# Kernel tuning notes

Hardware: AMD Instinct MI355X
Metric: run time of the kernel (lower is better)

The kernel has to match this reference:

```python
import jax, jax.numpy as jnp
import numpy as np

CM = 8        # channel_mult
EPS = 1e-5    # BatchNorm eps
NEG = 0.2     # LeakyReLU slope


def conv2d(x, w, stride, pad, b=None):
    y = jax.lax.conv_general_dilated(
        x, w, (stride, stride), [(pad, pad), (pad, pad)],
        dimension_numbers=('NCHW', 'OIHW', 'NCHW'))
    if b is not None:
        y = y + b[None, :, None, None]
    return y


def per_sample_conv(x, w, stride, pad):
    # x: [B,C,H,W], w: [B,O,C,kh,kw] -> per-sample conv, vmapped over batch
    f = lambda xi, wi: conv2d(xi[None], wi, stride, pad)[0]
    return jax.vmap(f)(x, w)


def batchnorm(x, g, b):
    # training-mode BN: batch statistics over (N,H,W)
    m = jnp.mean(x, axis=(0, 2, 3), keepdims=True)
    v = jnp.var(x, axis=(0, 2, 3), keepdims=True)
    return (x - m) * jax.lax.rsqrt(v + EPS) * g[None, :, None, None] + b[None, :, None, None]


def lrelu(x):
    return jnp.where(x >= 0, x, NEG * x)


def setup_inputs() -> dict:
    key = jax.random.key(0)
    ks = jax.random.split(key, 16)
    B, H, W = 16, 512, 512

    def rn(k, shape, fan_in):
        return jax.random.normal(k, shape, jnp.float32) * np.float32(1.0 / np.sqrt(fan_in))

    inp = {}
    inp['x'] = jax.random.normal(ks[0], (B, 3, H, W), jnp.float32)
    n_meta = 3 * (CM // 2) * 25 + CM * (CM * 2 // 2) * 25  # 300 + 1600 = 1900
    inp['conv_weights'] = jax.random.normal(ks[1], (B, n_meta), jnp.float32) * 0.05
    inp['w11'] = rn(ks[2], (CM // 2, 3, 5, 5), 3 * 25)
    inp['b11'] = jnp.zeros((CM // 2,), jnp.float32)
    inp['w12'] = rn(ks[3], (CM * 2 // 2, CM, 5, 5), CM * 25)
    inp['b12'] = jnp.zeros((CM * 2 // 2,), jnp.float32)
    inp['bn1_g'] = jnp.ones((CM * 2,), jnp.float32)
    inp['bn1_b'] = jnp.zeros((CM * 2,), jnp.float32)
    # conv2 stack: (in, out, kernel)
    chans = [(CM * 2, CM * 4, 5), (CM * 4, CM * 8, 5), (CM * 8, CM * 16, 3), (CM * 16, CM * 16, 3)]
    for i, (ci, co, k) in enumerate(chans, 1):
        inp[f'c2w{i}'] = rn(ks[3 + i], (co, ci, k, k), ci * k * k)
        inp[f'c2b{i}'] = jnp.zeros((co,), jnp.float32)
        inp[f'bn{i}g'] = jnp.ones((co,), jnp.float32)
        inp[f'bn{i}b'] = jnp.zeros((co,), jnp.float32)
    return inp


def reference(x, conv_weights, w11, b11, w12, b12, bn1_g, bn1_b,
              c2w1, c2b1, bn1g, bn1b, c2w2, c2b2, bn2g, bn2b,
              c2w3, c2b3, bn3g, bn3b, c2w4, c2b4, bn4g, bn4b):
    B, _, H, W = x.shape
    n1 = 3 * (CM // 2) * 25
    w1 = conv_weights[:, :n1].reshape(B, CM // 2, 3, 5, 5)
    w2 = conv_weights[:, n1:].reshape(B, CM * 2 // 2, CM, 5, 5)

    # meta layer 1: shared half + per-sample dynamic half
    xx = conv2d(x, w11, 1, 2, b11)                  # [B, cm/2, H, W]
    half = per_sample_conv(x, w1, 1, 2)             # [B, cm/2, H, W]
    h = lrelu(jnp.concatenate([xx, half], axis=1))  # [B, cm, H, W]

    # meta layer 2 (stride 2)
    xx = conv2d(h, w12, 2, 2, b12)                  # [B, cm, H/2, W/2]
    half = per_sample_conv(h, w2, 2, 2)             # [B, cm, H/2, W/2]
    h = lrelu(batchnorm(jnp.concatenate([xx, half], axis=1), bn1_g, bn1_b))

    # dense conv stack
    for w_, b_, g_, be_, p in [
        (c2w1, c2b1, bn1g, bn1b, 2),
        (c2w2, c2b2, bn2g, bn2b, 2),
        (c2w3, c2b3, bn3g, bn3b, 1),
        (c2w4, c2b4, bn4g, bn4b, 1),
    ]:
        h = lrelu(batchnorm(conv2d(h, w_, 2, p, b_), g_, be_))

    return h.reshape(-1, CM * 16, H // 32, W // 32)
```

## Files before the change

### kernel.cpp

```cpp
#include <hip/hip_runtime.h>


typedef __attribute__((ext_vector_type(8))) short short8v;
typedef __attribute__((ext_vector_type(4))) float float4v;
typedef __attribute__((ext_vector_type(4))) unsigned short ushort4v;
typedef unsigned short u16;

#define LRELU_NEG 0.2f
#define BN_EPS 1e-5f

__device__ __forceinline__ float bf2f(u16 u){ union{unsigned i; float f;} v; v.i=(unsigned)u<<16; return v.f; }
__device__ __forceinline__ u16 f2bf(float f){ unsigned x=__float_as_uint(f); x += 0x7FFFu + ((x>>16)&1u); return (u16)(x>>16); }
__device__ __forceinline__ float lrelu(float v){ return v<0.f? LRELU_NEG*v : v; }

__device__ __forceinline__ void packw(int i, const float* __restrict__ w, u16* __restrict__ dst,
                                      int IC, int OC, int KSZ, int CPR) {
  int kq = i & 31, oc = (i>>5) % OC, c = i/(OC*32);
  int ky = c / CPR, r = c % CPR;
  int kk = r*32 + kq; int kx = kk / IC, ic = kk % IC;
  float v = (kx < KSZ) ? w[(((size_t)oc*IC + ic)*KSZ + ky)*KSZ + kx] : 0.f;
  dst[i] = f2bf(v);
}

__global__ __launch_bounds__(256) void prep_all(
    const float* __restrict__ w11, const float* __restrict__ w12,
    const float* __restrict__ b12, const float* __restrict__ cw,
    const float* __restrict__ wc1, const float* __restrict__ wc2,
    const float* __restrict__ wc3, const float* __restrict__ wc4,
    u16* __restrict__ wl1d, u16* __restrict__ wl2m, float* __restrict__ bl2,
    u16* __restrict__ d1, u16* __restrict__ d2, u16* __restrict__ d3, u16* __restrict__ d4,
    u16* __restrict__ h1) {
  int i = blockIdx.x*256 + threadIdx.x;
  if (i < 16) {
    bl2[i] = (i<8)? b12[i] : 0.f;
  } else if (i < 49168) {
    int j = i - 16;
    int b = j / 3072, r = j % 3072;
    int c = r >> 9, r2 = r & 511;
    int row = r2 >> 5, kk = r2 & 31;
    int kx = kk >> 2, ic = kk & 3;
    int grp = row >> 3, oc = row & 7;
    int ky = c - grp;
    float v = 0.f;
    if (ic < 3 && kx < 5 && ky >= 0 && ky < 5)
      v = (oc < 4) ? w11[((oc*3+ic)*5+ky)*5+kx]
                   : cw[b*1900 + (oc-4)*75 + ic*25 + ky*5 + kx];
    wl1d[j] = f2bf(v);
  } else if (i < 131088) {
    int j = i - 49168;
    int kq = j & 31, oc = (j>>5) & 15, c = (j>>9) % 10, b = j / 5120;
    int ky = c >> 1, r = c & 1;
    int kk = r*32 + kq; int kx = kk >> 3, ic = kk & 7;
    float v = 0.f;
    if (kx < 5)
      v = (oc < 8) ? w12[((oc*8+ic)*5+ky)*5+kx]
                   : cw[b*1900 + 300 + ((oc-8)*8+ic)*25 + ky*5 + kx];
    wl2m[j] = f2bf(v);
  } else if (i < 196880) {
    int j = i - 131088;
    int b = j / 4112, p = j % 4112;
    int y, xx;
    if (p < 2064) { int r = p/516; y = (r<2)? r : 512+r; xx = p%516; }
    else          { int q = p-2064; int cidx = q&3; xx = (cidx<2)? cidx : 512+cidx; y = 2 + (q>>2); }
    short8v z = {0,0,0,0,0,0,0,0};
    *(short8v*)(h1 + ((((size_t)b*516 + y)*2 + (xx&1))*258 + (xx>>1))*8) = z;
  } else if (i < 484624) {
    int j = i - 196880;
    if (j < 15360) packw(j, wc1, d1, 16, 32, 5, 3);
    else if (j < 66560) packw(j-15360, wc2, d2, 32, 64, 5, 5);
    else if (j < 140288) packw(j-66560, wc3, d3, 64, 128, 3, 6);
    else packw(j-140288, wc4, d4, 128, 128, 3, 12);
  }
}

__global__ __launch_bounds__(256) void conv_l1(const float* __restrict__ x,
    const u16* __restrict__ wl1d, const float* __restrict__ b11,
    u16* __restrict__ h1) {
  __shared__ __align__(16) u16 sx[20*72*4 + 32];
  const int tid = threadIdx.x, b = blockIdx.z;
  const int x0 = (blockIdx.x & 7) * 64;
  const int r0 = (blockIdx.x >> 3) * 16;

  if (tid < 32) sx[20*72*4 + tid] = 0;

  const bool interior = (r0 >= 16) & (r0 <= 480) & (x0 >= 64) & (x0 <= 384);
  if (interior) {
    for (int e = tid; e < 360; e += 256) {
      int row = e / 18, cg = e % 18;
      size_t base = ((size_t)b*3*512 + r0 + row - 2)*512 + x0 + cg*4 - 4;
      float4v p0 = *(const float4v*)(x + base);
      float4v p1 = *(const float4v*)(x + base + 262144);
      float4v p2 = *(const float4v*)(x + base + 524288);
      short8v lo, hi;
#pragma unroll
      for (int j = 0; j < 2; j++) {
        lo[4*j+0] = (short)f2bf(p0[j]);   lo[4*j+1] = (short)f2bf(p1[j]);
        lo[4*j+2] = (short)f2bf(p2[j]);   lo[4*j+3] = 0;
        hi[4*j+0] = (short)f2bf(p0[j+2]); hi[4*j+1] = (short)f2bf(p1[j+2]);
        hi[4*j+2] = (short)f2bf(p2[j+2]); hi[4*j+3] = 0;
      }
      u16* dp = sx + (row*72 + cg*4)*4;
      *(short8v*)dp = lo;
      *(short8v*)(dp + 8) = hi;
    }
  } else {
    for (int e = tid; e < 1440; e += 256) {
      int row = e / 72, col = e % 72;
      int gy = r0 + row - 2, gx = x0 + col - 4;
      float v0 = 0.f, v1 = 0.f, v2 = 0.f;
      if (gy >= 0 && gy < 512 && gx >= 0 && gx < 512) {
        size_t base = ((size_t)b*3*512 + gy)*512 + gx;
        v0 = x[base]; v1 = x[base + 262144]; v2 = x[base + 524288];
      }
      ushort4 pk = {f2bf(v0), f2bf(v1), f2bf(v2), 0};
      *(ushort4*)(sx + e*4) = pk;
    }
  }
  __syncthreads();

  const int lane = tid & 63, w = tid >> 6;
  const int l15 = lane & 15, sub = lane >> 4;

  short8v Wf[6];
  const u16* wb = wl1d + (size_t)b*3072;
#pragma unroll
  for (int c = 0; c < 6; c++)
    Wf[c] = *(const short8v*)(wb + (c*16 + l15)*32 + sub*8);

  float bvv[4];
#pragma unroll
  for (int r = 0; r < 4; r++) bvv[r] = (sub & 1) ? 0.f : b11[r];

  const int colb = w*16 + l15;
  const int oc0 = (sub & 1) * 4;
  const int rsel = sub >> 1;
  const int x_out = x0 + colb + 2;
  const int xpar = x_out & 1, xp = x_out >> 1;

#pragma unroll
  for (int p = 0; p < 8; p++) {
    float4v acc = {0.f, 0.f, 0.f, 0.f};
#pragma unroll
    for (int c = 0; c < 6; c++) {
      const u16* ap = sx + (((2*p + c)*72 + colb + 2) << 2) + sub*8;
      union { unsigned long long q[2]; short8v v; } ua;
      ua.q[0] = *(const unsigned long long*)(ap);
      ua.q[1] = *(const unsigned long long*)(ap + 4);
      acc = __builtin_amdgcn_mfma_f32_16x16x32_bf16(Wf[c], ua.v, acc, 0, 0, 0);
    }
    ushort4v pk;
#pragma unroll
    for (int r = 0; r < 4; r++) pk[r] = f2bf(lrelu(acc[r] + bvv[r]));
    int outrow = r0 + 2*p + rsel;
    u16* dst = h1 + ((((size_t)b*516 + outrow + 2)*2 + xpar)*258 + xp)*8 + oc0;
    *(ushort4v*)dst = pk;
  }
}

#define LOADC(cc, Ax, Bx) do {                                                   \
    const int ky_ = (cc) / CPR, r_ = (cc) % CPR;                                 \
    const int kk0_ = r_*32 + sub*8;                                              \
    const int kx_ = kk0_ / IC, ico_ = kk0_ % IC;                                 \
    const int t_ = kx_ + PADOFF;                                                 \
    _Pragma("unroll") for (int n_ = 0; n_ < WN; n_++)                            \
      Bx[n_] = *(const short8v*)(wbase + ((size_t)(cc)*OC + oc0 + n_*16 + l15)*32 + sub*8); \
    _Pragma("unroll") for (int f_ = 0; f_ < WM; f_++) {                          \
      int iy_ = 2*oyf[f_] + ky_ + PADOFF;                                        \
      Ax[f_] = *(const short8v*)(inb + (((size_t)iy_*2 + (t_&1))*IPWH + axb[f_] + (t_>>1))*IC + ico_); \
    }                                                                            \
  } while(0)

#define MFMAC(Ax, Bx) do {                                                       \
    _Pragma("unroll") for (int f_ = 0; f_ < WM; f_++)                            \
      _Pragma("unroll") for (int n_ = 0; n_ < WN; n_++)                          \
        acc[f_][n_] = __builtin_amdgcn_mfma_f32_16x16x32_bf16(Ax[f_], Bx[n_], acc[f_][n_], 0, 0, 0); \
  } while(0)

template <int IC, int OC, int KSZ, int S, int P, int CPR, int NCH,
          int IPH, int IPW, int OWL, int OPH, int OPW,
          int WM, int WN, int WVM, int WVN, bool PERS>
__global__ __launch_bounds__(WVM*WVN*64) void conv_mfma(
    const u16* __restrict__ in, const u16* __restrict__ wmfma,
    const float* __restrict__ bias, u16* __restrict__ out,
    float2* __restrict__ part2) {
  constexpr int OW = 1 << OWL;
  constexpr int PADOFF = 2 - P;
  constexpr int IPWH = IPW / 2;
  constexpr int OPWH = OPW / 2;
  const int tid = threadIdx.x, lane = tid & 63;
  const int w = tid >> 6, wm = w % WVM, wn = w / WVM;
  const int l15 = lane & 15, sub = lane >> 4;
  const int b = blockIdx.z;
  const int px0 = blockIdx.x * (16*WM*WVM) + wm * (16*WM);
  const int oc0 = blockIdx.y * (16*WN*WVN) + wn * (16*WN);

  int oyf[WM], oxb[WM], axb[WM];
#pragma unroll
  for (int f = 0; f < WM; f++) {
    int p = px0 + f*16;
    oyf[f] = p >> OWL;
    oxb[f] = p & (OW-1);
    axb[f] = oxb[f] + l15;
  }
  const u16* inb = in + (size_t)b*IPH*IPW*IC;
  const u16* wbase = wmfma + (PERS ? (size_t)b*NCH*OC*32 : (size_t)0);

  float4v acc[WM][WN];
#pragma unroll
  for (int f = 0; f < WM; f++)
#pragma unroll
    for (int n = 0; n < WN; n++) acc[f][n] = (float4v){0.f,0.f,0.f,0.f};

  constexpr int NC = KSZ * CPR;
  short8v A0[WM], B0[WN], A1[WM], B1[WN];
  LOADC(0, A0, B0);
#pragma unroll
  for (int c = 0; c < NC; c += 2) {
    if (c + 1 < NC) LOADC(c + 1, A1, B1);
    MFMAC(A0, B0);
    if (c + 2 < NC) LOADC(c + 2, A0, B0);
    if (c + 1 < NC) MFMAC(A1, B1);
  }

  float s[WN], q[WN];
#pragma unroll
  for (int n = 0; n < WN; n++) { s[n] = 0.f; q[n] = 0.f; }
#pragma unroll
  for (int f = 0; f < WM; f++) {
    const int oxs = oxb[f] + sub*4;
    const size_t rowb2 = ((size_t)b*OPH + oyf[f] + 2)*2;
#pragma unroll
    for (int n = 0; n < WN; n++) {
      int oc = oc0 + n*16 + l15;
      float bv = bias[oc];
#pragma unroll
      for (int rr = 0; rr < 4; rr++) {
        float v = acc[f][n][rr] + bv;
        int x_out = oxs + rr + 2;
        out[((rowb2 + (x_out & 1))*OPWH + (x_out >> 1))*OC + oc] = f2bf(v);
        s[n] += v; q[n] += v*v;
      }
    }
  }
#pragma unroll
  for (int n = 0; n < WN; n++) {
    s[n] += __shfl_xor(s[n], 16); s[n] += __shfl_xor(s[n], 32);
    q[n] += __shfl_xor(q[n], 16); q[n] += __shfl_xor(q[n], 32);
  }
  __shared__ float sred[WVM*WVN][WN][16][2];
  if (sub == 0) {
#pragma unroll
    for (int n = 0; n < WN; n++) { sred[w][n][l15][0] = s[n]; sred[w][n][l15][1] = q[n]; }
  }
  __syncthreads();
  const int NBp = gridDim.x * gridDim.z;
  const int pb = blockIdx.z * gridDim.x + blockIdx.x;
  const int tot = WVN*WN*16;
  if (tid < tot) {
    int c16 = tid & 15, n = (tid >> 4) % WN, wn2 = tid / (16*WN);
    float S_ = 0.f, Q_ = 0.f;
    for (int wm2 = 0; wm2 < WVM; wm2++) {
      S_ += sred[wn2*WVM + wm2][n][c16][0];
      Q_ += sred[wn2*WVM + wm2][n][c16][1];
    }
    int c = blockIdx.y*(16*WN*WVN) + wn2*(16*WN) + n*16 + c16;
    part2[(size_t)c*NBp + pb] = make_float2(S_, Q_);
  }
}

__global__ void bn_stage2(const float2* __restrict__ part2, const float* __restrict__ g,
                          const float* __restrict__ bb, float* __restrict__ stats,
                          int NBp, float invN) {
  int c = blockIdx.x;
  float s = 0.f, q = 0.f;
  for (int i = threadIdx.x; i < NBp; i += 64) {
    float2 p = part2[(size_t)c*NBp + i];
    s += p.x; q += p.y;
  }
  for (int o = 32; o > 0; o >>= 1) { s += __shfl_down(s, o); q += __shfl_down(q, o); }
  if (threadIdx.x == 0) {
    float m = s * invN;
    float var = q * invN - m*m;
    float sc = g[c] * rsqrtf(var + BN_EPS);
    stats[2*c] = sc;
    stats[2*c+1] = bb[c] - m*sc;
  }
}

template <int C, int PH, int PW, int HH, int WW>
__global__ __launch_bounds__(256) void bn_fin(u16* __restrict__ y, const float* __restrict__ stats,
                                              int total8) {
  int i = blockIdx.x*256 + threadIdx.x;
  if (i >= total8) return;
  size_t e = (size_t)i*8;
  int c0 = (int)(e & (C-1));
  int px = (int)(e / C);
  int xp = px % (PW/2);
  int t2 = px / (PW/2);
  int yy = (t2 >> 1) % PH;
  bool interior = (yy >= 2) & (yy < 2+HH) & (xp >= 1) & (xp <= WW/2);
  short8v u = *(short8v*)(y + e);
  short8v o;
#pragma unroll
  for (int j = 0; j < 8; j++) {
    float v = bf2f((u16)u[j]) * stats[2*(c0+j)] + stats[2*(c0+j)+1];
    o[j] = interior ? (short)f2bf(lrelu(v)) : (short)0;
  }
  *(short8v*)(y + e) = o;
}

__global__ __launch_bounds__(256) void out_k(const u16* __restrict__ y6,
                                             const float* __restrict__ stats,
                                             float* __restrict__ out) {
  int i = blockIdx.x*256 + threadIdx.x;
  if (i >= 131072) return;
  size_t e = (size_t)i*4;
  int c0 = (int)(e & 127);
  int px = (int)(e >> 7);
  int loc = px & 255, b = px >> 8;
  int y = loc >> 4, x = loc & 15;
  int xi = x + 2;
  const u16* src = y6 + ((((size_t)b*20 + y + 2)*2 + (xi & 1))*10 + (xi >> 1))*128 + c0;
  ushort4 u = *(const ushort4*)src;
  float vv[4] = {bf2f(u.x), bf2f(u.y), bf2f(u.z), bf2f(u.w)};
#pragma unroll
  for (int j = 0; j < 4; j++) {
    int c = c0 + j;
    float v = vv[j] * stats[2*c] + stats[2*c+1];
    out[(((size_t)b*128 + c) << 8) + loc] = lrelu(v);
  }
}

extern "C" void kernel_launch(void* const* d_in, const int* in_sizes, int n_in,
                              void* d_out, int out_size, void* d_ws, size_t ws_size,
                              hipStream_t stream) {
  const float* x    = (const float*)d_in[0];
  const float* cw   = (const float*)d_in[1];
  const float* w11  = (const float*)d_in[2];
  const float* b11  = (const float*)d_in[3];
  const float* w12  = (const float*)d_in[4];
  const float* b12  = (const float*)d_in[5];
  const float* bn1g = (const float*)d_in[6];
  const float* bn1b = (const float*)d_in[7];
  const float* c2w[4] = {(const float*)d_in[8], (const float*)d_in[12],
                         (const float*)d_in[16], (const float*)d_in[20]};
  const float* c2b[4] = {(const float*)d_in[9], (const float*)d_in[13],
                         (const float*)d_in[17], (const float*)d_in[21]};
  const float* bng[4] = {(const float*)d_in[10], (const float*)d_in[14],
                         (const float*)d_in[18], (const float*)d_in[22]};
  const float* bnb[4] = {(const float*)d_in[11], (const float*)d_in[15],
                         (const float*)d_in[19], (const float*)d_in[23]};

  char* ws = (char*)d_ws;
  u16* h1   = (u16*)(ws);
  u16* y3   = (u16*)(ws);
  u16* y4   = (u16*)(ws + 17842176);
  u16* y5   = (u16*)(ws + 27312128);
  u16* y6   = (u16*)(ws + 32620544);
  u16* yT2  = (u16*)(ws + 68158464);
  u16* wl2m = (u16*)(ws + 102769664);
  float* bl2    = (float*)(ws + 102933504);
  float2* part2 = (float2*)(ws + 102933568);
  float* stats2 = (float*)(ws + 103457856);
  float* stats3 = stats2 + 32;
  float* stats4 = stats3 + 64;
  float* stats5 = stats4 + 128;
  float* stats6 = stats5 + 256;
  u16* wl1d = (u16*)(ws + 103460800);
  u16* wS1  = (u16*)(ws + 103559104);
  u16* wS2  = (u16*)(ws + 103589824);
  u16* wS3  = (u16*)(ws + 103692224);
  u16* wS4  = (u16*)(ws + 103839680);

  prep_all<<<1894, 256, 0, stream>>>(w11, w12, b12, cw,
                                     c2w[0], c2w[1], c2w[2], c2w[3],
                                     wl1d, wl2m, bl2, wS1, wS2, wS3, wS4, h1);

  conv_l1<<<dim3(256, 1, 16), 256, 0, stream>>>(x, wl1d, b11, h1);

  conv_mfma<8,16,5,2,2, 2,10, 516,516, 8, 260,260, 4,1,4,1, true>
      <<<dim3(256,1,16), 256, 0, stream>>>(h1, wl2m, bl2, yT2, part2);

  bn_stage2<<<16, 64, 0, stream>>>(part2, bn1g, bn1b, stats2, 4096, 1.f/1048576.f);
  bn_fin<16,260,260,256,256><<<8450, 256, 0, stream>>>(yT2, stats2, 2163200);

  conv_mfma<16,32,5,2,2, 3,15, 260,260, 7, 132,132, 2,2,4,1, false>
      <<<dim3(128,1,16), 256, 0, stream>>>(yT2, wS1, c2b[0], y3, part2);
  bn_stage2<<<32, 64, 0, stream>>>(part2, bng[0], bnb[0], stats3, 2048, 1.f/262144.f);
  bn_fin<32,132,132,128,128><<<4356, 256, 0, stream>>>(y3, stats3, 1115136);

  conv_mfma<32,64,5,2,2, 5,25, 132,132, 6, 68,68, 2,2,2,2, false>
      <<<dim3(64,1,16), 256, 0, stream>>>(y3, wS2, c2b[1], y4, part2);
  bn_stage2<<<64, 64, 0, stream>>>(part2, bng[1], bnb[1], stats4, 1024, 1.f/65536.f);
  bn_fin<64,68,68,64,64><<<2312, 256, 0, stream>>>(y4, stats4, 591872);

  conv_mfma<64,128,3,2,1, 6,18, 68,68, 5, 36,36, 2,2,2,2, false>
      <<<dim3(16,2,16), 256, 0, stream>>>(y4, wS3, c2b[2], y5, part2);
  bn_stage2<<<128, 64, 0, stream>>>(part2, bng[2], bnb[2], stats5, 256, 1.f/16384.f);
  bn_fin<128,36,36,32,32><<<1296, 256, 0, stream>>>(y5, stats5, 331776);

  conv_mfma<128,128,3,2,1, 12,36, 36,36, 4, 20,20, 2,2,1,2, false>
      <<<dim3(8,2,16), 128, 0, stream>>>(y5, wS4, c2b[3], y6, part2);
  bn_stage2<<<128, 64, 0, stream>>>(part2, bng[3], bnb[3], stats6, 128, 1.f/4096.f);

  out_k<<<512, 256, 0, stream>>>(y6, stats6, (float*)d_out);
}
```

Before: 252.6 us.

## Stage conv input halos in swizzled LDS and retile conv launches

The strided conv kernel now cooperatively copies the block's input rows (with halo) into shared memory using an XOR swizzle, then reads the A fragments from LDS instead of issuing a direct global load per fragment. This targets redundant global/L2 traffic from overlapping receptive fields. The explicit double-buffered register prefetch is dropped in favour of a simple loop. The first layer uses smaller per-wave tiles with twice as many blocks, the last layer uses four N-waves in one block, and the partials buffer moves to a larger offset. LDS use and the added barrier may reduce occupancy, and losing the manual prefetch may expose latency.

Result: slower. 283.1 us (+12.1%).

```diff
diff --git a/kernel.cpp b/kernel.cpp
--- a/kernel.cpp
+++ b/kernel.cpp
@@ -157,28 +157,9 @@
   }
 }
 
-#define LOADC(cc, Ax, Bx) do {                                                   \
-    const int ky_ = (cc) / CPR, r_ = (cc) % CPR;                                 \
-    const int kk0_ = r_*32 + sub*8;                                              \
-    const int kx_ = kk0_ / IC, ico_ = kk0_ % IC;                                 \
-    const int t_ = kx_ + PADOFF;                                                 \
-    _Pragma("unroll") for (int n_ = 0; n_ < WN; n_++)                            \
-      Bx[n_] = *(const short8v*)(wbase + ((size_t)(cc)*OC + oc0 + n_*16 + l15)*32 + sub*8); \
-    _Pragma("unroll") for (int f_ = 0; f_ < WM; f_++) {                          \
-      int iy_ = 2*oyf[f_] + ky_ + PADOFF;                                        \
-      Ax[f_] = *(const short8v*)(inb + (((size_t)iy_*2 + (t_&1))*IPWH + axb[f_] + (t_>>1))*IC + ico_); \
-    }                                                                            \
-  } while(0)
-
-#define MFMAC(Ax, Bx) do {                                                       \
-    _Pragma("unroll") for (int f_ = 0; f_ < WM; f_++)                            \
-      _Pragma("unroll") for (int n_ = 0; n_ < WN; n_++)                          \
-        acc[f_][n_] = __builtin_amdgcn_mfma_f32_16x16x32_bf16(Ax[f_], Bx[n_], acc[f_][n_], 0, 0, 0); \
-  } while(0)
-
-template <int IC, int OC, int KSZ, int S, int P, int CPR, int NCH,
+template <int IC, int OC, int KSZ, int P, int CPR, int NCH,
           int IPH, int IPW, int OWL, int OPH, int OPW,
-          int WM, int WN, int WVM, int WVN, bool PERS>
+          int WM, int WN, int WVM, int WVN, int NOY, int SWZM, bool PERS>
 __global__ __launch_bounds__(WVM*WVN*64) void conv_mfma(
     const u16* __restrict__ in, const u16* __restrict__ wmfma,
     const float* __restrict__ bias, u16* __restrict__ out,
@@ -187,22 +168,50 @@
   constexpr int PADOFF = 2 - P;
   constexpr int IPWH = IPW / 2;
   constexpr int OPWH = OPW / 2;
+  constexpr int NROWS = 2*(NOY-1) + KSZ;
+  constexpr int KXMAX = (32*CPR - 8) / IC;
+  constexpr int THALF = (KXMAX + PADOFF) >> 1;
+  constexpr int PXBLK = 16*WM*WVM;
+  constexpr int PXROW = PXBLK / NOY;
+  constexpr int XHSPAN = PXROW + THALF + 1;
+  constexpr int XHP = (XHSPAN + 1) & ~1;
+  constexpr int ICG = IC / 8;
+  constexpr int NG = NROWS * 2 * XHSPAN * ICG;
+  constexpr int NC = KSZ * CPR;
+  constexpr int NTHR = WVM*WVN*64;
+
+  __shared__ __align__(16) u16 sx[NROWS*2*XHP*IC];
+
   const int tid = threadIdx.x, lane = tid & 63;
   const int w = tid >> 6, wm = w % WVM, wn = w / WVM;
   const int l15 = lane & 15, sub = lane >> 4;
   const int b = blockIdx.z;
-  const int px0 = blockIdx.x * (16*WM*WVM) + wm * (16*WM);
+  const int px0 = blockIdx.x * PXBLK;
   const int oc0 = blockIdx.y * (16*WN*WVN) + wn * (16*WN);
-
-  int oyf[WM], oxb[WM], axb[WM];
+  const int oy_min = px0 >> OWL;
+  const int ox0 = px0 & (OW-1);
+  const int iy0 = 2*oy_min + PADOFF;
+
+  const u16* inb = in + (size_t)b*IPH*IPW*IC;
+
+  for (int g = tid; g < NG; g += NTHR) {
+    int gc = g % ICG;
+    int xh = (g / ICG) % XHSPAN;
+    int rp = g / (ICG * XHSPAN);
+    int par = rp & 1, row = rp >> 1;
+    const u16* src = inb + (((size_t)(iy0+row)*2 + par)*IPWH + ox0 + xh)*IC + gc*8;
+    int db = ((((row*2+par)*XHP + xh)*IC + gc*8) << 1) ^ ((xh & SWZM) << 4);
+    *(short8v*)((char*)sx + db) = *(const short8v*)src;
+  }
+  __syncthreads();
+
+  int oyl[WM], oxl[WM];
 #pragma unroll
   for (int f = 0; f < WM; f++) {
-    int p = px0 + f*16;
-    oyf[f] = p >> OWL;
-    oxb[f] = p & (OW-1);
-    axb[f] = oxb[f] + l15;
-  }
-  const u16* inb = in + (size_t)b*IPH*IPW*IC;
+    int p = px0 + wm*(16*WM) + f*16;
+    oyl[f] = (p >> OWL) - oy_min;
+    oxl[f] = (p & (OW-1)) - ox0;
+  }
   const u16* wbase = wmfma + (PERS ? (size_t)b*NCH*OC*32 : (size_t)0);
 
   float4v acc[WM][WN];
@@ -211,15 +220,29 @@
 #pragma unroll
     for (int n = 0; n < WN; n++) acc[f][n] = (float4v){0.f,0.f,0.f,0.f};
 
-  constexpr int NC = KSZ * CPR;
-  short8v A0[WM], B0[WN], A1[WM], B1[WN];
-  LOADC(0, A0, B0);
-#pragma unroll
-  for (int c = 0; c < NC; c += 2) {
-    if (c + 1 < NC) LOADC(c + 1, A1, B1);
-    MFMAC(A0, B0);
-    if (c + 2 < NC) LOADC(c + 2, A0, B0);
-    if (c + 1 < NC) MFMAC(A1, B1);
+#pragma unroll
+  for (int c = 0; c < NC; c++) {
+    const int ky = c / CPR, r = c % CPR;
+    const int kk0 = r*32 + sub*8;
+    const int kx = kk0 / IC, ico = kk0 % IC;
+    const int t = kx + PADOFF;
+    short8v B[WN];
+#pragma unroll
+    for (int n = 0; n < WN; n++)
+      B[n] = *(const short8v*)(wbase + ((size_t)c*OC + oc0 + n*16 + l15)*32 + sub*8);
+    short8v A[WM];
+#pragma unroll
+    for (int f = 0; f < WM; f++) {
+      int rowl = 2*oyl[f] + ky;
+      int xh_l = oxl[f] + l15 + (t >> 1);
+      int ab = ((((rowl*2 + (t&1))*XHP + xh_l)*IC + ico) << 1) ^ ((xh_l & SWZM) << 4);
+      A[f] = *(const short8v*)((const char*)sx + ab);
+    }
+#pragma unroll
+    for (int f = 0; f < WM; f++)
+#pragma unroll
+      for (int n = 0; n < WN; n++)
+        acc[f][n] = __builtin_amdgcn_mfma_f32_16x16x32_bf16(A[f], B[n], acc[f][n], 0, 0, 0);
   }
 
   float s[WN], q[WN];
@@ -227,8 +250,8 @@
   for (int n = 0; n < WN; n++) { s[n] = 0.f; q[n] = 0.f; }
 #pragma unroll
   for (int f = 0; f < WM; f++) {
-    const int oxs = oxb[f] + sub*4;
-    const size_t rowb2 = ((size_t)b*OPH + oyf[f] + 2)*2;
+    const int oxs = (oxl[f] + ox0) + sub*4;
+    const size_t rowb2 = ((size_t)b*OPH + (oyl[f] + oy_min) + 2)*2;
 #pragma unroll
     for (int n = 0; n < WN; n++) {
       int oc = oc0 + n*16 + l15;
@@ -360,7 +383,6 @@
   u16* yT2  = (u16*)(ws + 68158464);
   u16* wl2m = (u16*)(ws + 102769664);
   float* bl2    = (float*)(ws + 102933504);
-  float2* part2 = (float2*)(ws + 102933568);
   float* stats2 = (float*)(ws + 103457856);
   float* stats3 = stats2 + 32;
   float* stats4 = stats3 + 64;
@@ -371,6 +393,7 @@
   u16* wS2  = (u16*)(ws + 103589824);
   u16* wS3  = (u16*)(ws + 103692224);
   u16* wS4  = (u16*)(ws + 103839680);
+  float2* part2 = (float2*)(ws + 104857600);
 
   prep_all<<<1894, 256, 0, stream>>>(w11, w12, b12, cw,
                                      c2w[0], c2w[1], c2w[2], c2w[3],
@@ -378,29 +401,29 @@
 
   conv_l1<<<dim3(256, 1, 16), 256, 0, stream>>>(x, wl1d, b11, h1);
 
-  conv_mfma<8,16,5,2,2, 2,10, 516,516, 8, 260,260, 4,1,4,1, true>
-      <<<dim3(256,1,16), 256, 0, stream>>>(h1, wl2m, bl2, yT2, part2);
-
-  bn_stage2<<<16, 64, 0, stream>>>(part2, bn1g, bn1b, stats2, 4096, 1.f/1048576.f);
+  conv_mfma<8,16,5,2, 2,10, 516,516, 8, 260,260, 2,1,4,1, 1,0, true>
+      <<<dim3(512,1,16), 256, 0, stream>>>(h1, wl2m, bl2, yT2, part2);
+
+  bn_stage2<<<16, 64, 0, stream>>>(part2, bn1g, bn1b, stats2, 8192, 1.f/1048576.f);
   bn_fin<16,260,260,256,256><<<8450, 256, 0, stream>>>(yT2, stats2, 2163200);
 
-  conv_mfma<16,32,5,2,2, 3,15, 260,260, 7, 132,132, 2,2,4,1, false>
+  conv_mfma<16,32,5,2, 3,15, 260,260, 7, 132,132, 2,2,4,1, 1,1, false>
       <<<dim3(128,1,16), 256, 0, stream>>>(yT2, wS1, c2b[0], y3, part2);
   bn_stage2<<<32, 64, 0, stream>>>(part2, bng[0], bnb[0], stats3, 2048, 1.f/262144.f);
   bn_fin<32,132,132,128,128><<<4356, 256, 0, stream>>>(y3, stats3, 1115136);
 
-  conv_mfma<32,64,5,2,2, 5,25, 132,132, 6, 68,68, 2,2,2,2, false>
+  conv_mfma<32,64,5,2, 5,25, 132,132, 6, 68,68, 2,2,2,2, 1,3, false>
       <<<dim3(64,1,16), 256, 0, stream>>>(y3, wS2, c2b[1], y4, part2);
   bn_stage2<<<64, 64, 0, stream>>>(part2, bng[1], bnb[1], stats4, 1024, 1.f/65536.f);
   bn_fin<64,68,68,64,64><<<2312, 256, 0, stream>>>(y4, stats4, 591872);
 
-  conv_mfma<64,128,3,2,1, 6,18, 68,68, 5, 36,36, 2,2,2,2, false>
+  conv_mfma<64,128,3,1, 6,18, 68,68, 5, 36,36, 2,2,2,2, 2,7, false>
       <<<dim3(16,2,16), 256, 0, stream>>>(y4, wS3, c2b[2], y5, part2);
   bn_stage2<<<128, 64, 0, stream>>>(part2, bng[2], bnb[2], stats5, 256, 1.f/16384.f);
   bn_fin<128,36,36,32,32><<<1296, 256, 0, stream>>>(y5, stats5, 331776);
 
-  conv_mfma<128,128,3,2,1, 12,36, 36,36, 4, 20,20, 2,2,1,2, false>
-      <<<dim3(8,2,16), 128, 0, stream>>>(y5, wS4, c2b[3], y6, part2);
+  conv_mfma<128,128,3,1, 12,36, 36,36, 4, 20,20, 2,2,1,4, 2,7, false>
+      <<<dim3(8,1,16), 256, 0, stream>>>(y5, wS4, c2b[3], y6, part2);
   bn_stage2<<<128, 64, 0, stream>>>(part2, bng[3], bnb[3], stats6, 128, 1.f/4096.f);
 
   out_k<<<512, 256, 0, stream>>>(y6, stats6, (float*)d_out);
```
